# Optimization experiments

Hardware: AMD Instinct MI355X
Metric: run time of the kernel (lower is better)

Reference implementation:

```python
import jax, jax.numpy as jnp
import numpy as np

N_POINTS = 262144
SP_FEAT = 128
HIDDEN = 64
EMBED = 256
NUM_SP = 4096
NUM_SP2 = 256
PAD_LIMIT = 64
MASK_RATIO = 0.6


def setup_inputs() -> dict:
    key = jax.random.key(0)
    ks = jax.random.split(key, 6)
    x = jax.random.normal(ks[0], (N_POINTS, SP_FEAT), jnp.float32)
    # point -> superpoint ids, sorted; force every superpoint non-empty
    idx10 = jax.random.randint(ks[1], (N_POINTS,), 0, NUM_SP)
    idx10 = jnp.sort(idx10.at[:NUM_SP].set(jnp.arange(NUM_SP))).astype(jnp.int32)
    # superpoint -> higher superpoint, balanced (16 per group, < PAD_LIMIT), sorted
    idx21 = ((jnp.arange(NUM_SP) * NUM_SP2) // NUM_SP).astype(jnp.int32)
    # deterministic mask: exactly int(NUM_SP * MASK_RATIO) superpoints masked
    mask_num = int(NUM_SP * MASK_RATIO)
    perm = jax.random.permutation(ks[2], NUM_SP)
    is_masked = jnp.zeros((NUM_SP,), bool).at[perm[:mask_num]].set(True)
    W1 = jax.random.normal(ks[3], (SP_FEAT, HIDDEN), jnp.float32) / np.sqrt(SP_FEAT).astype(np.float32)
    b1 = jnp.zeros((HIDDEN,), jnp.float32)
    W2 = jax.random.normal(ks[4], (HIDDEN, EMBED), jnp.float32) / np.sqrt(HIDDEN).astype(np.float32)
    b2 = jnp.zeros((EMBED,), jnp.float32)
    return {
        "full_features": x,
        "full_super_indices_10": idx10,
        "full_super_indices_21": idx21,
        "is_masked": is_masked,
        "W1": W1, "b1": b1, "W2": W2, "b2": b2,
    }


def _pad_scatter(tokens, idx21, flag):
    # tokens: [NUM_SP, C]; idx21 sorted sp->sp2 ids; flag: [NUM_SP] bool.
    # rank of each flagged superpoint within its sp2 group (in sp order)
    f = flag.astype(jnp.int32)
    cum = jnp.cumsum(f)                                            # inclusive global cumsum
    per_group = jax.ops.segment_sum(f, idx21, num_segments=NUM_SP2)
    prefix = jnp.concatenate([jnp.zeros((1,), jnp.int32), jnp.cumsum(per_group)[:-1]])
    rank = cum - 1 - prefix[idx21]                                 # 0-based slot within group
    slot = jnp.where(flag, rank, PAD_LIMIT)                        # PAD_LIMIT -> dropped
    out = jnp.zeros((NUM_SP2, PAD_LIMIT, tokens.shape[-1]), tokens.dtype)
    return out.at[idx21, slot].set(tokens, mode="drop")


def reference(full_features, full_super_indices_10, full_super_indices_21,
              is_masked, W1, b1, W2, b2):
    # per-point 2-layer MLP (gather is implicit: MLP is pointwise), then segment max
    h = jax.nn.relu(full_features @ W1 + b1)                       # [N, HIDDEN]
    h = jax.nn.relu(h @ W2 + b2)                                   # [N, EMBED]
    tok = jax.ops.segment_max(h, full_super_indices_10, num_segments=NUM_SP)  # [NUM_SP, EMBED]
    remain_tokens = _pad_scatter(tok, full_super_indices_21, ~is_masked)      # [NUM_SP2, PAD, EMBED]
    mask_tokens = _pad_scatter(tok, full_super_indices_21, is_masked)         # [NUM_SP2, PAD, EMBED]
    return (remain_tokens, mask_tokens)
```

## Files before the change

kernel.cpp:

```cpp
#include <hip/hip_runtime.h>
#include <hip/hip_bf16.h>

#define N_POINTS 262144
#define SP_FEAT 128
#define HIDDEN 64
#define EMBED 256
#define NUM_SP 4096
#define NUM_SP2 256
#define PAD_LIMIT 64

typedef __bf16 bf16x8 __attribute__((ext_vector_type(8)));
typedef float floatx4 __attribute__((ext_vector_type(4)));
using bf16 = __hip_bfloat16;

__global__ void prep_kernel(const float* __restrict__ W1, const float* __restrict__ W2,
                            bf16* __restrict__ W1t, bf16* __restrict__ W2t) {
    int i = blockIdx.x * blockDim.x + threadIdx.x;
    if (i < HIDDEN * SP_FEAT) {
        int n = i >> 7;
        int k = i & 127;
        W1t[i] = __float2bfloat16(W1[k * HIDDEN + n]);
    }
    int j = i - HIDDEN * SP_FEAT;
    if (j >= 0 && j < EMBED * HIDDEN) {
        int n = j >> 6;
        int k = j & 63;
        W2t[j] = __float2bfloat16(W2[k * EMBED + n]);
    }
}

__global__ __launch_bounds__(256) void mlp_segmax_kernel(
    const float* __restrict__ X, const int* __restrict__ idx10,
    const bf16* __restrict__ W1t, const float* __restrict__ b1,
    const bf16* __restrict__ W2t, const float* __restrict__ b2,
    int* __restrict__ tok_bits)
{
    __shared__ __align__(16) bf16 Xs[64][136];
    __shared__ __align__(16) bf16 H1s[64][72];
    __shared__ int sIdx[64];

    const int tid  = threadIdx.x;
    const int lane = tid & 63;
    const int w    = tid >> 6;
    const int l15  = lane & 15;
    const int quad = lane >> 4;
    const int m0   = blockIdx.x * 64;

    bf16x8 bw1[4];
    {
        const bf16* p = W1t + (16 * w + l15) * SP_FEAT + quad * 8;
#pragma unroll
        for (int ks = 0; ks < 4; ++ks)
            bw1[ks] = *(const bf16x8*)(p + 32 * ks);
    }
    bf16x8 bf2[4][2];
#pragma unroll
    for (int tn = 0; tn < 4; ++tn) {
        const bf16* p = W2t + (64 * w + 16 * tn + l15) * HIDDEN + quad * 8;
#pragma unroll
        for (int ks = 0; ks < 2; ++ks)
            bf2[tn][ks] = *(const bf16x8*)(p + 32 * ks);
    }
    float b2f[4];
#pragma unroll
    for (int tn = 0; tn < 4; ++tn)
        b2f[tn] = b2[64 * w + 16 * tn + l15];
    const float b1v = b1[16 * w + l15];

#pragma unroll
    for (int i = 0; i < 4; ++i) {
        int c   = tid + 256 * i;
        int row = c >> 4;
        int cc  = (c & 15) * 8;
        const float* src = X + (size_t)(m0 + row) * SP_FEAT + cc;
        float4 u0 = *(const float4*)src;
        float4 u1 = *(const float4*)(src + 4);
        union { bf16x8 v; bf16 h[8]; } u;
        u.h[0] = __float2bfloat16(u0.x); u.h[1] = __float2bfloat16(u0.y);
        u.h[2] = __float2bfloat16(u0.z); u.h[3] = __float2bfloat16(u0.w);
        u.h[4] = __float2bfloat16(u1.x); u.h[5] = __float2bfloat16(u1.y);
        u.h[6] = __float2bfloat16(u1.z); u.h[7] = __float2bfloat16(u1.w);
        *(bf16x8*)(&Xs[row][cc]) = u.v;
    }
    if (tid < 64) sIdx[tid] = idx10[m0 + tid];
    __syncthreads();

    floatx4 zero4 = {0.f, 0.f, 0.f, 0.f};
    floatx4 acc1[4] = {zero4, zero4, zero4, zero4};
#pragma unroll
    for (int ks = 0; ks < 4; ++ks) {
        int k = ks * 32 + quad * 8;
#pragma unroll
        for (int tm = 0; tm < 4; ++tm) {
            bf16x8 a = *(bf16x8*)(&Xs[16 * tm + l15][k]);
            acc1[tm] = __builtin_amdgcn_mfma_f32_16x16x32_bf16(a, bw1[ks], acc1[tm], 0, 0, 0);
        }
    }
#pragma unroll
    for (int tm = 0; tm < 4; ++tm) {
#pragma unroll
        for (int r = 0; r < 4; ++r) {
            float v = acc1[tm][r] + b1v;
            v = v > 0.f ? v : 0.f;
            H1s[16 * tm + quad * 4 + r][16 * w + l15] = __float2bfloat16(v);
        }
    }
    __syncthreads();

    floatx4 acc2[4][4];
#pragma unroll
    for (int tm = 0; tm < 4; ++tm)
#pragma unroll
        for (int tn = 0; tn < 4; ++tn) acc2[tm][tn] = zero4;
#pragma unroll
    for (int tm = 0; tm < 4; ++tm) {
        bf16x8 a0 = *(bf16x8*)(&H1s[16 * tm + l15][quad * 8]);
        bf16x8 a1 = *(bf16x8*)(&H1s[16 * tm + l15][32 + quad * 8]);
#pragma unroll
        for (int tn = 0; tn < 4; ++tn) {
            acc2[tm][tn] = __builtin_amdgcn_mfma_f32_16x16x32_bf16(a0, bf2[tn][0], acc2[tm][tn], 0, 0, 0);
            acc2[tm][tn] = __builtin_amdgcn_mfma_f32_16x16x32_bf16(a1, bf2[tn][1], acc2[tm][tn], 0, 0, 0);
        }
    }

#pragma unroll
    for (int tn = 0; tn < 4; ++tn) {
        int col = 64 * w + 16 * tn + l15;
        float cur = 0.f;
        int cursp = -1;
#pragma unroll
        for (int tm = 0; tm < 4; ++tm) {
            int r0 = 16 * tm + quad * 4;
#pragma unroll
            for (int r = 0; r < 4; ++r) {
                float v = acc2[tm][tn][r] + b2f[tn];
                v = v > 0.f ? v : 0.f;
                int sp = sIdx[r0 + r];
                if (sp == cursp) {
                    cur = fmaxf(cur, v);
                } else {
                    if (cursp >= 0)
                        atomicMax(&tok_bits[cursp * EMBED + col], __float_as_int(cur));
                    cursp = sp;
                    cur = v;
                }
            }
        }
        atomicMax(&tok_bits[cursp * EMBED + col], __float_as_int(cur));
    }
}

__global__ __launch_bounds__(256) void scatter_kernel(
    const float* __restrict__ tok, const int* __restrict__ idx21,
    const void* __restrict__ is_masked, float* __restrict__ out)
{
    __shared__ int lspR[PAD_LIMIT], lspM[PAD_LIMIT];
    __shared__ int cnt[2];
    __shared__ int enc;
    const int g = blockIdx.x;
    const int tid = threadIdx.x;

    if (tid == 0) enc = 0;
    __syncthreads();
    {
        const unsigned char* mb = (const unsigned char*)is_masked;
        int local = 0;
        for (int p = tid; p < NUM_SP; p += 256)
            if ((p & 3) && mb[p]) local = 1;
        if (local) atomicOr(&enc, 1);
    }
    __syncthreads();
    const int e = enc;

    if (tid == 0) {
        const unsigned char* mb = (const unsigned char*)is_masked;
        const int* mi = (const int*)is_masked;
        int a = 0, b = NUM_SP;
        while (a < b) { int m = (a + b) >> 1; if (idx21[m] < g) a = m + 1; else b = m; }
        int lo = a;
        b = NUM_SP;
        while (a < b) { int m = (a + b) >> 1; if (idx21[m] < g + 1) a = m + 1; else b = m; }
        int hi = a;
        int nR = 0, nM = 0;
        for (int s = lo; s < hi; ++s) {
            int msk = e ? (int)mb[s] : mi[s];
            if (msk) { if (nM < PAD_LIMIT) lspM[nM] = s; nM++; }
            else     { if (nR < PAD_LIMIT) lspR[nR] = s; nR++; }
        }
        cnt[0] = nR < PAD_LIMIT ? nR : PAD_LIMIT;
        cnt[1] = nM < PAD_LIMIT ? nM : PAD_LIMIT;
    }
    __syncthreads();
    const int nR = cnt[0], nM = cnt[1];
    float* outR = out + (size_t)g * PAD_LIMIT * EMBED;
    float* outM = out + (size_t)NUM_SP2 * PAD_LIMIT * EMBED + (size_t)g * PAD_LIMIT * EMBED;
    for (int r = 0; r < nR; ++r)
        outR[r * EMBED + tid] = tok[lspR[r] * EMBED + tid];
    for (int r = 0; r < nM; ++r)
        outM[r * EMBED + tid] = tok[lspM[r] * EMBED + tid];
}

extern "C" void kernel_launch(void* const* d_in, const int* in_sizes, int n_in,
                              void* d_out, int out_size, void* d_ws, size_t ws_size,
                              hipStream_t stream) {
    (void)in_sizes; (void)n_in; (void)ws_size;
    const float* X       = (const float*)d_in[0];
    const int* idx10     = (const int*)d_in[1];
    const int* idx21     = (const int*)d_in[2];
    const void* is_masked= (const void*)d_in[3];
    const float* W1      = (const float*)d_in[4];
    const float* b1      = (const float*)d_in[5];
    const float* W2      = (const float*)d_in[6];
    const float* b2      = (const float*)d_in[7];
    float* out           = (float*)d_out;

    char* ws   = (char*)d_ws;
    float* tok = (float*)ws;
    bf16* W1t  = (bf16*)(ws + (size_t)NUM_SP * EMBED * 4);
    bf16* W2t  = W1t + HIDDEN * SP_FEAT;

    hipMemsetAsync(tok, 0, (size_t)NUM_SP * EMBED * sizeof(float), stream);
    hipMemsetAsync(d_out, 0, (size_t)out_size * sizeof(float), stream);

    prep_kernel<<<(HIDDEN * SP_FEAT + EMBED * HIDDEN + 255) / 256, 256, 0, stream>>>(
        W1, W2, W1t, W2t);
    mlp_segmax_kernel<<<N_POINTS / 64, 256, 0, stream>>>(
        X, idx10, W1t, b1, W2t, b2, (int*)tok);
    scatter_kernel<<<NUM_SP2, 256, 0, stream>>>(tok, idx21, is_masked, out);
}
```

Measured before the change: 257.1 us.

## Map one block per superpoint, compute segment max in registers, drop atomics and memsets

The MLP kernel now launches one block per superpoint, using segment start offsets found by binary search in the prep kernel. It loops over 64-row tiles, keeps a running max in registers, and writes each token row once, which removes the global atomicMax traffic and both memsets. Group ranking moves into a separate single-block kernel that writes inverse-index tables. The scatter kernel is split into 8 parts per group and also writes the zero padding. Segment sizes average 64 points, so uneven segments leave many tiles partly filled, padded by re-reading the last row. That wastes MFMA work and risks load imbalance across blocks.

```diff
diff --git a/kernel.cpp b/kernel.cpp
--- a/kernel.cpp
+++ b/kernel.cpp
@@ -14,217 +14,233 @@
 using bf16 = __hip_bfloat16;
 
 __global__ void prep_kernel(const float* __restrict__ W1, const float* __restrict__ W2,
-                            bf16* __restrict__ W1t, bf16* __restrict__ W2t) {
+                            const int* __restrict__ idx10,
+                            bf16* __restrict__ W1t, bf16* __restrict__ W2t,
+                            int* __restrict__ start) {
     int i = blockIdx.x * blockDim.x + threadIdx.x;
     if (i < HIDDEN * SP_FEAT) {
-        int n = i >> 7;
-        int k = i & 127;
+        int n = i >> 7, k = i & 127;
         W1t[i] = __float2bfloat16(W1[k * HIDDEN + n]);
-    }
-    int j = i - HIDDEN * SP_FEAT;
-    if (j >= 0 && j < EMBED * HIDDEN) {
-        int n = j >> 6;
-        int k = j & 63;
+    } else if (i < HIDDEN * SP_FEAT + EMBED * HIDDEN) {
+        int j = i - HIDDEN * SP_FEAT;
+        int n = j >> 6, k = j & 63;
         W2t[j] = __float2bfloat16(W2[k * EMBED + n]);
-    }
+    } else if (i <= HIDDEN * SP_FEAT + EMBED * HIDDEN + NUM_SP) {
+        int s = i - (HIDDEN * SP_FEAT + EMBED * HIDDEN);
+        if (s == NUM_SP) { start[s] = N_POINTS; return; }
+        int a = 0, b = N_POINTS;
+        while (a < b) { int m = (a + b) >> 1; if (idx10[m] < s) a = m + 1; else b = m; }
+        start[s] = a;
+    }
+}
+
+__global__ __launch_bounds__(256) void rank_kernel(
+    const int* __restrict__ idx21, const void* __restrict__ is_masked,
+    int* __restrict__ invR, int* __restrict__ invM) {
+    __shared__ int encS;
+    const int tid = threadIdx.x;
+    if (tid == 0) encS = 0;
+    __syncthreads();
+    const unsigned char* mb = (const unsigned char*)is_masked;
+    const int* mi = (const int*)is_masked;
+    int local = 0;
+    for (int p = tid; p < NUM_SP; p += 256)
+        if ((p & 3) && mb[p]) local = 1;
+    if (local) atomicOr(&encS, 1);
+    __syncthreads();
+    const int e = encS;
+
+    const int g = tid;
+    int a = 0, b = NUM_SP;
+    while (a < b) { int m = (a + b) >> 1; if (idx21[m] < g) a = m + 1; else b = m; }
+    int lo = a;
+    b = NUM_SP;
+    while (a < b) { int m = (a + b) >> 1; if (idx21[m] < g + 1) a = m + 1; else b = m; }
+    int hi = a;
+    int nR = 0, nM = 0;
+    for (int s = lo; s < hi; ++s) {
+        int msk = e ? (int)mb[s] : mi[s];
+        if (msk) { if (nM < PAD_LIMIT) invM[g * PAD_LIMIT + nM] = s; nM++; }
+        else     { if (nR < PAD_LIMIT) invR[g * PAD_LIMIT + nR] = s; nR++; }
+    }
+    for (int r = nR; r < PAD_LIMIT; ++r) invR[g * PAD_LIMIT + r] = -1;
+    for (int r = nM; r < PAD_LIMIT; ++r) invM[g * PAD_LIMIT + r] = -1;
 }
 
 __global__ __launch_bounds__(256) void mlp_segmax_kernel(
-    const float* __restrict__ X, const int* __restrict__ idx10,
+    const float* __restrict__ X, const int* __restrict__ start,
     const bf16* __restrict__ W1t, const float* __restrict__ b1,
     const bf16* __restrict__ W2t, const float* __restrict__ b2,
-    int* __restrict__ tok_bits)
+    float* __restrict__ tok)
 {
     __shared__ __align__(16) bf16 Xs[64][136];
     __shared__ __align__(16) bf16 H1s[64][72];
-    __shared__ int sIdx[64];
+    __shared__ float tokS[EMBED];
 
     const int tid  = threadIdx.x;
     const int lane = tid & 63;
     const int w    = tid >> 6;
     const int l15  = lane & 15;
     const int quad = lane >> 4;
-    const int m0   = blockIdx.x * 64;
+    const int s    = blockIdx.x;
+
+    const int s0 = start[s];
+    int cnt = start[s + 1] - s0;
+    if (cnt < 1) cnt = 1;
+    const int ntiles = (cnt + 63) >> 6;
 
     bf16x8 bw1[4];
     {
         const bf16* p = W1t + (16 * w + l15) * SP_FEAT + quad * 8;
 #pragma unroll
-        for (int ks = 0; ks < 4; ++ks)
-            bw1[ks] = *(const bf16x8*)(p + 32 * ks);
+        for (int ks = 0; ks < 4; ++ks) bw1[ks] = *(const bf16x8*)(p + 32 * ks);
     }
     bf16x8 bf2[4][2];
 #pragma unroll
     for (int tn = 0; tn < 4; ++tn) {
         const bf16* p = W2t + (64 * w + 16 * tn + l15) * HIDDEN + quad * 8;
 #pragma unroll
-        for (int ks = 0; ks < 2; ++ks)
-            bf2[tn][ks] = *(const bf16x8*)(p + 32 * ks);
+        for (int ks = 0; ks < 2; ++ks) bf2[tn][ks] = *(const bf16x8*)(p + 32 * ks);
     }
     float b2f[4];
 #pragma unroll
-    for (int tn = 0; tn < 4; ++tn)
-        b2f[tn] = b2[64 * w + 16 * tn + l15];
+    for (int tn = 0; tn < 4; ++tn) b2f[tn] = b2[64 * w + 16 * tn + l15];
     const float b1v = b1[16 * w + l15];
 
-#pragma unroll
-    for (int i = 0; i < 4; ++i) {
-        int c   = tid + 256 * i;
-        int row = c >> 4;
-        int cc  = (c & 15) * 8;
-        const float* src = X + (size_t)(m0 + row) * SP_FEAT + cc;
-        float4 u0 = *(const float4*)src;
-        float4 u1 = *(const float4*)(src + 4);
-        union { bf16x8 v; bf16 h[8]; } u;
-        u.h[0] = __float2bfloat16(u0.x); u.h[1] = __float2bfloat16(u0.y);
-        u.h[2] = __float2bfloat16(u0.z); u.h[3] = __float2bfloat16(u0.w);
-        u.h[4] = __float2bfloat16(u1.x); u.h[5] = __float2bfloat16(u1.y);
-        u.h[6] = __float2bfloat16(u1.z); u.h[7] = __float2bfloat16(u1.w);
-        *(bf16x8*)(&Xs[row][cc]) = u.v;
-    }
-    if (tid < 64) sIdx[tid] = idx10[m0 + tid];
+    floatx4 zero4 = {0.f, 0.f, 0.f, 0.f};
+    floatx4 macc[4][4];
+#pragma unroll
+    for (int tm = 0; tm < 4; ++tm)
+#pragma unroll
+        for (int tn = 0; tn < 4; ++tn)
+#pragma unroll
+            for (int r = 0; r < 4; ++r) macc[tm][tn][r] = -3e38f;
+
+    for (int t = 0; t < ntiles; ++t) {
+        __syncthreads();
+#pragma unroll
+        for (int i = 0; i < 4; ++i) {
+            int c   = tid + 256 * i;
+            int row = c >> 4;
+            int cc  = (c & 15) * 8;
+            int pr  = t * 64 + row;
+            if (pr >= cnt) pr = cnt - 1;
+            const float* src = X + (size_t)(s0 + pr) * SP_FEAT + cc;
+            float4 u0 = *(const float4*)src;
+            float4 u1 = *(const float4*)(src + 4);
+            union { bf16x8 v; bf16 h[8]; } u;
+            u.h[0] = __float2bfloat16(u0.x); u.h[1] = __float2bfloat16(u0.y);
+            u.h[2] = __float2bfloat16(u0.z); u.h[3] = __float2bfloat16(u0.w);
+            u.h[4] = __float2bfloat16(u1.x); u.h[5] = __float2bfloat16(u1.y);
+            u.h[6] = __float2bfloat16(u1.z); u.h[7] = __float2bfloat16(u1.w);
+            *(bf16x8*)(&Xs[row][cc]) = u.v;
+        }
+        __syncthreads();
+
+        floatx4 acc1[4] = {zero4, zero4, zero4, zero4};
+#pragma unroll
+        for (int ks = 0; ks < 4; ++ks) {
+            int k = ks * 32 + quad * 8;
+#pragma unroll
+            for (int tm = 0; tm < 4; ++tm) {
+                bf16x8 a = *(bf16x8*)(&Xs[16 * tm + l15][k]);
+                acc1[tm] = __builtin_amdgcn_mfma_f32_16x16x32_bf16(a, bw1[ks], acc1[tm], 0, 0, 0);
+            }
+        }
+#pragma unroll
+        for (int tm = 0; tm < 4; ++tm) {
+#pragma unroll
+            for (int r = 0; r < 4; ++r) {
+                float v = acc1[tm][r] + b1v;
+                v = v > 0.f ? v : 0.f;
+                H1s[16 * tm + quad * 4 + r][16 * w + l15] = __float2bfloat16(v);
+            }
+        }
+        __syncthreads();
+
+#pragma unroll
+        for (int tm = 0; tm < 4; ++tm) {
+            bf16x8 a0 = *(bf16x8*)(&H1s[16 * tm + l15][quad * 8]);
+            bf16x8 a1 = *(bf16x8*)(&H1s[16 * tm + l15][32 + quad * 8]);
+#pragma unroll
+            for (int tn = 0; tn < 4; ++tn) {
+                floatx4 acc = zero4;
+                acc = __builtin_amdgcn_mfma_f32_16x16x32_bf16(a0, bf2[tn][0], acc, 0, 0, 0);
+                acc = __builtin_amdgcn_mfma_f32_16x16x32_bf16(a1, bf2[tn][1], acc, 0, 0, 0);
+#pragma unroll
+                for (int r = 0; r < 4; ++r)
+                    macc[tm][tn][r] = fmaxf(macc[tm][tn][r], acc[r]);
+            }
+        }
+    }
+
+#pragma unroll
+    for (int tn = 0; tn < 4; ++tn) {
+        float bst = -3e38f;
+#pragma unroll
+        for (int tm = 0; tm < 4; ++tm)
+#pragma unroll
+            for (int r = 0; r < 4; ++r) bst = fmaxf(bst, macc[tm][tn][r]);
+        bst = fmaxf(bst, __shfl_xor(bst, 16, 64));
+        bst = fmaxf(bst, __shfl_xor(bst, 32, 64));
+        float v = bst + b2f[tn];
+        v = v > 0.f ? v : 0.f;
+        if (quad == 0) tokS[64 * w + 16 * tn + l15] = v;
+    }
     __syncthreads();
-
-    floatx4 zero4 = {0.f, 0.f, 0.f, 0.f};
-    floatx4 acc1[4] = {zero4, zero4, zero4, zero4};
-#pragma unroll
-    for (int ks = 0; ks < 4; ++ks) {
-        int k = ks * 32 + quad * 8;
-#pragma unroll
-        for (int tm = 0; tm < 4; ++tm) {
-            bf16x8 a = *(bf16x8*)(&Xs[16 * tm + l15][k]);
-            acc1[tm] = __builtin_amdgcn_mfma_f32_16x16x32_bf16(a, bw1[ks], acc1[tm], 0, 0, 0);
-        }
-    }
-#pragma unroll
-    for (int tm = 0; tm < 4; ++tm) {
-#pragma unroll
-        for (int r = 0; r < 4; ++r) {
-            float v = acc1[tm][r] + b1v;
-            v = v > 0.f ? v : 0.f;
-            H1s[16 * tm + quad * 4 + r][16 * w + l15] = __float2bfloat16(v);
-        }
-    }
-    __syncthreads();
-
-    floatx4 acc2[4][4];
-#pragma unroll
-    for (int tm = 0; tm < 4; ++tm)
-#pragma unroll
-        for (int tn = 0; tn < 4; ++tn) acc2[tm][tn] = zero4;
-#pragma unroll
-    for (int tm = 0; tm < 4; ++tm) {
-        bf16x8 a0 = *(bf16x8*)(&H1s[16 * tm + l15][quad * 8]);
-        bf16x8 a1 = *(bf16x8*)(&H1s[16 * tm + l15][32 + quad * 8]);
-#pragma unroll
-        for (int tn = 0; tn < 4; ++tn) {
-            acc2[tm][tn] = __builtin_amdgcn_mfma_f32_16x16x32_bf16(a0, bf2[tn][0], acc2[tm][tn], 0, 0, 0);
-            acc2[tm][tn] = __builtin_amdgcn_mfma_f32_16x16x32_bf16(a1, bf2[tn][1], acc2[tm][tn], 0, 0, 0);
-        }
-    }
-
-#pragma unroll
-    for (int tn = 0; tn < 4; ++tn) {
-        int col = 64 * w + 16 * tn + l15;
-        float cur = 0.f;
-        int cursp = -1;
-#pragma unroll
-        for (int tm = 0; tm < 4; ++tm) {
-            int r0 = 16 * tm + quad * 4;
-#pragma unroll
-            for (int r = 0; r < 4; ++r) {
-                float v = acc2[tm][tn][r] + b2f[tn];
-                v = v > 0.f ? v : 0.f;
-                int sp = sIdx[r0 + r];
-                if (sp == cursp) {
-                    cur = fmaxf(cur, v);
-                } else {
-                    if (cursp >= 0)
-                        atomicMax(&tok_bits[cursp * EMBED + col], __float_as_int(cur));
-                    cursp = sp;
-                    cur = v;
-                }
-            }
-        }
-        atomicMax(&tok_bits[cursp * EMBED + col], __float_as_int(cur));
-    }
+    tok[(size_t)s * EMBED + tid] = tokS[tid];
 }
 
 __global__ __launch_bounds__(256) void scatter_kernel(
-    const float* __restrict__ tok, const int* __restrict__ idx21,
-    const void* __restrict__ is_masked, float* __restrict__ out)
+    const float* __restrict__ tok, const int* __restrict__ invR,
+    const int* __restrict__ invM, float* __restrict__ out)
 {
-    __shared__ int lspR[PAD_LIMIT], lspM[PAD_LIMIT];
-    __shared__ int cnt[2];
-    __shared__ int enc;
-    const int g = blockIdx.x;
-    const int tid = threadIdx.x;
-
-    if (tid == 0) enc = 0;
-    __syncthreads();
-    {
-        const unsigned char* mb = (const unsigned char*)is_masked;
-        int local = 0;
-        for (int p = tid; p < NUM_SP; p += 256)
-            if ((p & 3) && mb[p]) local = 1;
-        if (local) atomicOr(&enc, 1);
-    }
-    __syncthreads();
-    const int e = enc;
-
-    if (tid == 0) {
-        const unsigned char* mb = (const unsigned char*)is_masked;
-        const int* mi = (const int*)is_masked;
-        int a = 0, b = NUM_SP;
-        while (a < b) { int m = (a + b) >> 1; if (idx21[m] < g) a = m + 1; else b = m; }
-        int lo = a;
-        b = NUM_SP;
-        while (a < b) { int m = (a + b) >> 1; if (idx21[m] < g + 1) a = m + 1; else b = m; }
-        int hi = a;
-        int nR = 0, nM = 0;
-        for (int s = lo; s < hi; ++s) {
-            int msk = e ? (int)mb[s] : mi[s];
-            if (msk) { if (nM < PAD_LIMIT) lspM[nM] = s; nM++; }
-            else     { if (nR < PAD_LIMIT) lspR[nR] = s; nR++; }
-        }
-        cnt[0] = nR < PAD_LIMIT ? nR : PAD_LIMIT;
-        cnt[1] = nM < PAD_LIMIT ? nM : PAD_LIMIT;
-    }
-    __syncthreads();
-    const int nR = cnt[0], nM = cnt[1];
+    const int g    = blockIdx.x >> 3;
+    const int part = blockIdx.x & 7;
+    const int tid  = threadIdx.x;
     float* outR = out + (size_t)g * PAD_LIMIT * EMBED;
     float* outM = out + (size_t)NUM_SP2 * PAD_LIMIT * EMBED + (size_t)g * PAD_LIMIT * EMBED;
-    for (int r = 0; r < nR; ++r)
-        outR[r * EMBED + tid] = tok[lspR[r] * EMBED + tid];
-    for (int r = 0; r < nM; ++r)
-        outM[r * EMBED + tid] = tok[lspM[r] * EMBED + tid];
+#pragma unroll
+    for (int rr = 0; rr < 16; ++rr) {
+        int row = part * 16 + rr;
+        if (row < PAD_LIMIT) {
+            int sp = invR[g * PAD_LIMIT + row];
+            float v = (sp >= 0) ? tok[(size_t)sp * EMBED + tid] : 0.f;
+            outR[row * EMBED + tid] = v;
+        } else {
+            int r = row - PAD_LIMIT;
+            int sp = invM[g * PAD_LIMIT + r];
+            float v = (sp >= 0) ? tok[(size_t)sp * EMBED + tid] : 0.f;
+            outM[r * EMBED + tid] = v;
+        }
+    }
 }
 
 extern "C" void kernel_launch(void* const* d_in, const int* in_sizes, int n_in,
                               void* d_out, int out_size, void* d_ws, size_t ws_size,
                               hipStream_t stream) {
-    (void)in_sizes; (void)n_in; (void)ws_size;
-    const float* X       = (const float*)d_in[0];
-    const int* idx10     = (const int*)d_in[1];
-    const int* idx21     = (const int*)d_in[2];
-    const void* is_masked= (const void*)d_in[3];
-    const float* W1      = (const float*)d_in[4];
-    const float* b1      = (const float*)d_in[5];
-    const float* W2      = (const float*)d_in[6];
-    const float* b2      = (const float*)d_in[7];
-    float* out           = (float*)d_out;
-
-    char* ws   = (char*)d_ws;
-    float* tok = (float*)ws;
-    bf16* W1t  = (bf16*)(ws + (size_t)NUM_SP * EMBED * 4);
-    bf16* W2t  = W1t + HIDDEN * SP_FEAT;
-
-    hipMemsetAsync(tok, 0, (size_t)NUM_SP * EMBED * sizeof(float), stream);
-    hipMemsetAsync(d_out, 0, (size_t)out_size * sizeof(float), stream);
-
-    prep_kernel<<<(HIDDEN * SP_FEAT + EMBED * HIDDEN + 255) / 256, 256, 0, stream>>>(
-        W1, W2, W1t, W2t);
-    mlp_segmax_kernel<<<N_POINTS / 64, 256, 0, stream>>>(
-        X, idx10, W1t, b1, W2t, b2, (int*)tok);
-    scatter_kernel<<<NUM_SP2, 256, 0, stream>>>(tok, idx21, is_masked, out);
-}
+    (void)in_sizes; (void)n_in; (void)ws_size; (void)out_size;
+    const float* X        = (const float*)d_in[0];
+    const int* idx10      = (const int*)d_in[1];
+    const int* idx21      = (const int*)d_in[2];
+    const void* is_masked = (const void*)d_in[3];
+    const float* W1       = (const float*)d_in[4];
+    const float* b1       = (const float*)d_in[5];
+    const float* W2       = (const float*)d_in[6];
+    const float* b2       = (const float*)d_in[7];
+    float* out            = (float*)d_out;
+
+    char* ws    = (char*)d_ws;
+    float* tok  = (float*)ws;
+    bf16* W1t   = (bf16*)(ws + (size_t)NUM_SP * EMBED * 4);
+    bf16* W2t   = W1t + HIDDEN * SP_FEAT;
+    int*  start = (int*)((char*)(W2t + EMBED * HIDDEN));
+    int*  invR  = start + (NUM_SP + 2);
+    int*  invM  = invR + NUM_SP2 * PAD_LIMIT;
+
+    const int prep_n = HIDDEN * SP_FEAT + EMBED * HIDDEN + NUM_SP + 1;
+    prep_kernel<<<(prep_n + 255) / 256, 256, 0, stream>>>(W1, W2, idx10, W1t, W2t, start);
+    rank_kernel<<<1, 256, 0, stream>>>(idx21, is_masked, invR, invM);
+    mlp_segmax_kernel<<<NUM_SP, 256, 0, stream>>>(X, start, W1t, b1, W2t, b2, tok);
+    scatter_kernel<<<NUM_SP2 * 8, 256, 0, stream>>>(tok, invR, invM, out);
+}
```

Measured after the change: 265.4 us. +3.2%, slower.
